# Optimization experiments

Hardware: AMD Instinct MI355X
Metric: run time of the kernel (lower is better)

The kernel has to match this reference:

```python
import jax, jax.numpy as jnp
import numpy as np

FREQ_RES = 100.0 / 256.0
NUM_FILTERS = 6
_CFG = [(0.5, 4.0), (4.0, 8.0), (8.0, 12.0), (12.0, 16.0), (16.0, 24.0), (24.0, 30.0)]
BANDS = [(int(a / FREQ_RES), int(b / FREQ_RES)) for a, b in _CFG]  # (start_bin, end_bin)


def _interp_idx(n_src, n_dst):
    # torch F.interpolate bilinear, align_corners=False, along last dim (T dim is identity since same size)
    j = np.arange(n_dst)
    src = np.maximum((j + 0.5) * n_src / n_dst - 0.5, 0.0)
    x0 = np.floor(src).astype(np.int32)
    x1 = np.minimum(x0 + 1, n_src - 1)
    w = (src - x0).astype(np.float32)
    return x0, x1, w


def _gelu(x):
    return jax.nn.gelu(x, approximate=False)


def _forward(spec, centers, widths, gains, align_w, align_b, fc1_w, fc1_b, fc2_w, fc2_b,
             band_gain, gate_w, gate_b, proj_w, proj_b, bn_gamma, bn_beta, bn_mean, bn_var):
    B, C, T, F = spec.shape
    N = NUM_FILTERS
    band_feats = []
    for i, (s, e) in enumerate(BANDS):
        nb = e - s + 1
        sl = spec[:, :, :, s:e + 1]                       # [B,C,T,nb]
        mu = jax.nn.softplus(centers[i]) + s              # [C,N]
        mu = jnp.clip(mu, s, s + nb - 1)
        std = jnp.clip(jax.nn.softplus(widths[i]) + 1e-3, 0.5, 2.0 * nb / N)
        freqs = jnp.arange(nb, dtype=spec.dtype)          # relative bins [nb]
        g = jnp.exp(-0.5 * ((freqs[None, None, :] - mu[:, :, None]) / std[:, :, None]) ** 2)  # [C,N,nb]
        w = gains[i][:, :, None] * g / (g.sum(-1, keepdims=True) + 1e-6)
        filt = jnp.einsum('bctf,cnf->bctn', sl, w)        # [B,C,T,N]
        aligned = jnp.einsum('bctn,dc->bdtn', filt, align_w[i]) + align_b[i][None, :, None, None]
        band_feats.append(aligned)
    band_stack = jnp.stack(band_feats, axis=1)            # [B,6,C,T,N]
    nb_bands = band_stack.shape[1]
    x = band_stack.reshape(B, nb_bands * C, T, N)
    h = _gelu(jnp.einsum('bktn,ok->botn', x, fc1_w) + fc1_b[None, :, None, None])
    attn = jnp.einsum('botn,ko->bktn', h, fc2_w) + fc2_b[None, :, None, None]
    attn = jax.nn.softmax(attn.reshape(B, nb_bands, C, T, N), axis=1)  # softmax over bands
    band_stack = band_stack * attn * band_gain[None, :, None, None, None]
    enhanced = jnp.zeros_like(spec)
    for i, (s, e) in enumerate(BANDS):
        nb = e - s + 1
        narrow = band_stack[:, i]                         # [B,C,T,N]
        x0, x1, wl = _interp_idx(NUM_FILTERS, nb)
        wl = jnp.asarray(wl, dtype=spec.dtype)
        bf = narrow[..., x0] * (1.0 - wl) + narrow[..., x1] * wl   # [B,C,T,nb]
        enhanced = enhanced.at[:, :, :, s:e + 1].add(bf)
    residual = enhanced - spec
    gate = jax.nn.sigmoid(jnp.einsum('bctf,dc->bdtf', residual, gate_w) + gate_b[None, :, None, None])
    enhanced2 = spec + gate * residual
    y = jnp.einsum('bctf,dc->bdtf', enhanced2, proj_w) + proj_b[None, :, None, None]
    y = (y - bn_mean[None, :, None, None]) / jnp.sqrt(bn_var[None, :, None, None] + 1e-5)
    y = y * bn_gamma[None, :, None, None] + bn_beta[None, :, None, None]
    return _gelu(y)


def setup_inputs() -> dict:
    key = jax.random.key(0)
    ks = jax.random.split(key, 8)
    B, C, T, F, N = 64, 3, 3000, 103, NUM_FILTERS
    spec = jax.random.normal(ks[0], (B, C, T, F), dtype=jnp.float32)
    centers = jnp.stack([jnp.broadcast_to(jnp.linspace(a, b, N, dtype=jnp.float32) / FREQ_RES, (C, N)) for a, b in _CFG])
    widths = jnp.stack([jnp.full((C, N), (b - a) / N / FREQ_RES, dtype=jnp.float32) for a, b in _CFG])
    gains = jnp.ones((6, C, N), jnp.float32)
    align_w = jax.random.normal(ks[1], (6, C, C), dtype=jnp.float32) / np.sqrt(C)
    align_b = jax.random.normal(ks[2], (6, C), dtype=jnp.float32) * 0.02
    inter = 2 * C
    fc1_w = jax.random.normal(ks[3], (inter, 6 * C), dtype=jnp.float32) / np.sqrt(6 * C)
    fc1_b = jnp.zeros((inter,), jnp.float32)
    fc2_w = jax.random.normal(ks[4], (6 * C, inter), dtype=jnp.float32) / np.sqrt(inter)
    fc2_b = jnp.zeros((6 * C,), jnp.float32)
    band_gain = jnp.ones((6,), jnp.float32)
    gate_w = jax.random.normal(ks[5], (C, C), dtype=jnp.float32) / np.sqrt(C)
    gate_b = jnp.zeros((C,), jnp.float32)
    proj_w = jax.random.normal(ks[6], (C, C), dtype=jnp.float32) / np.sqrt(C)
    proj_b = jnp.zeros((C,), jnp.float32)
    bn_gamma = jnp.ones((C,), jnp.float32)
    bn_beta = jnp.zeros((C,), jnp.float32)
    bn_mean = jnp.zeros((C,), jnp.float32)
    bn_var = jnp.ones((C,), jnp.float32)
    return {"spec": spec, "centers": centers, "widths": widths, "gains": gains,
            "align_w": align_w, "align_b": align_b, "fc1_w": fc1_w, "fc1_b": fc1_b,
            "fc2_w": fc2_w, "fc2_b": fc2_b, "band_gain": band_gain,
            "gate_w": gate_w, "gate_b": gate_b, "proj_w": proj_w, "proj_b": proj_b,
            "bn_gamma": bn_gamma, "bn_beta": bn_beta, "bn_mean": bn_mean, "bn_var": bn_var}


def reference(spec, centers, widths, gains, align_w, align_b, fc1_w, fc1_b, fc2_w, fc2_b,
              band_gain, gate_w, gate_b, proj_w, proj_b, bn_gamma, bn_beta, bn_mean, bn_var):
    return _forward(spec, centers, widths, gains, align_w, align_b, fc1_w, fc1_b, fc2_w, fc2_b,
                    band_gain, gate_w, gate_b, proj_w, proj_b, bn_gamma, bn_beta, bn_mean, bn_var)
```

## Files before the change

kernel.cpp:

```cpp
#include <hip/hip_runtime.h>
#include <math.h>

namespace {

constexpr int C_ = 3, T_ = 3000, F_ = 103, NB_ = 6;
constexpr int TT = 20;
constexpr int BS[NB_]  = {1, 10, 20, 30, 40, 61};
constexpr int BNB[NB_] = {10, 11, 11, 11, 22, 16};
constexpr int BOF[NB_] = {0, 10, 21, 32, 43, 65};
constexpr int SPF = 81;
constexpr int PLANE = T_ * F_;
constexpr int SEC = 2064;
constexpr int POOLN = 6320;

__device__ __forceinline__ float softplus_(float x) {
  return fmaxf(x, 0.0f) + log1pf(expf(-fabsf(x)));
}
__device__ __forceinline__ float sigmoid_(float z) {
  return 1.0f / (1.0f + __expf(-z));
}
__device__ __forceinline__ float gelu_(float x) {
  return x * sigmoid_(1.595769122f * x * (1.0f + 0.044715f * x * x));
}

__global__ __launch_bounds__(256)
void sleepband_kernel(const float* __restrict__ spec,
                      const float* __restrict__ centers,
                      const float* __restrict__ widths,
                      const float* __restrict__ gains,
                      const float* __restrict__ align_w,
                      const float* __restrict__ align_b,
                      const float* __restrict__ fc1_w,
                      const float* __restrict__ fc1_b,
                      const float* __restrict__ fc2_w,
                      const float* __restrict__ fc2_b,
                      const float* __restrict__ band_gain,
                      const float* __restrict__ gate_w,
                      const float* __restrict__ gate_b,
                      const float* __restrict__ proj_w,
                      const float* __restrict__ proj_b,
                      const float* __restrict__ bn_gamma,
                      const float* __restrict__ bn_beta,
                      const float* __restrict__ bn_mean,
                      const float* __restrict__ bn_var,
                      float* __restrict__ out)
{
  __shared__ __align__(16) float sPool[POOLN];
  __shared__ float sBand[TT][109];
  __shared__ float sAw[54], sAb[18], sF1[108], sF1b[6], sF2[108], sF2b[18],
                   sBg[6], sGw[9], sGb[3], sPw[9], sPb[3], sBnS[3], sBnO[3];

  const int tid = threadIdx.x;
  const int t0  = blockIdx.x * TT;
  const int b   = blockIdx.y;

  float* sW = sPool + C_ * TT * SPF;

  const float* specB = spec + (size_t)b * C_ * PLANE;
  for (int li = tid; li < C_ * TT * SPF; li += 256) {
    int c   = li / (TT * SPF);
    int rem = li - c * (TT * SPF);
    int tt  = rem / SPF;
    int f   = rem - tt * SPF;
    sPool[li] = specB[(size_t)c * PLANE + (size_t)(t0 + tt) * F_ + f];
  }

  if (tid < 54)  sAw[tid]  = align_w[tid];
  if (tid < 18)  sAb[tid]  = align_b[tid];
  if (tid < 108) sF1[tid]  = fc1_w[tid];
  if (tid < 6)   sF1b[tid] = fc1_b[tid];
  if (tid < 108) sF2[tid]  = fc2_w[tid];
  if (tid < 18)  sF2b[tid] = fc2_b[tid];
  if (tid < 6)   sBg[tid]  = band_gain[tid];
  if (tid < 9)   sGw[tid]  = gate_w[tid];
  if (tid < 3)   sGb[tid]  = gate_b[tid];
  if (tid < 9)   sPw[tid]  = proj_w[tid];
  if (tid < 3)   sPb[tid]  = proj_b[tid];
  if (tid < 3) {
    float sc = bn_gamma[tid] / sqrtf(bn_var[tid] + 1e-5f);
    sBnS[tid] = sc;
    sBnO[tid] = bn_beta[tid] - bn_mean[tid] * sc;
  }

  if (tid >= 128 && tid < 128 + 108) {
    int q = tid - 128;
    int i = q / 18;
    int p = q - i * 18;
    int s = BS[i], nb = BNB[i];
    float mu = softplus_(centers[q]) + (float)s;
    mu = fminf(fmaxf(mu, (float)s), (float)(s + nb - 1));
    float sd = softplus_(widths[q]) + 0.001f;
    sd = fminf(fmaxf(sd, 0.5f), 2.0f * (float)nb / 6.0f);
    float sum = 0.0f;
    for (int f = 0; f < nb; ++f) {
      float d = ((float)f - mu) / sd;
      sum += __expf(-0.5f * d * d);
    }
    float sc = gains[q] / (sum + 1e-6f);
    float* wrow = &sW[BOF[i] * 18 + p * nb];
    for (int f = 0; f < nb; ++f) {
      float d = ((float)f - mu) / sd;
      wrow[f] = sc * __expf(-0.5f * d * d);
    }
  }
  __syncthreads();

  for (int task = tid; task < 18 * TT; task += 256) {
    int p  = task / TT;
    int tt = task - p * TT;
    int c  = p / 6;
    int n  = p - c * 6;
    const float* srowb = &sPool[(c * TT + tt) * SPF];
    #pragma unroll
    for (int i = 0; i < NB_; ++i) {
      const float* wrow = &sW[BOF[i] * 18 + p * BNB[i]];
      const float* srow = srowb + BS[i];
      float acc = 0.0f;
      #pragma unroll
      for (int f = 0; f < BNB[i]; ++f) acc += srow[f] * wrow[f];
      sBand[tt][(i * 3 + c) * 6 + n] = acc;
    }
  }
  __syncthreads();

  if (tid < 6 * TT) {
    int n  = tid / TT;
    int tt = tid - n * TT;
    float al[18];
    #pragma unroll
    for (int i = 0; i < 6; ++i) {
      float f0 = sBand[tt][(i * 3 + 0) * 6 + n];
      float f1 = sBand[tt][(i * 3 + 1) * 6 + n];
      float f2 = sBand[tt][(i * 3 + 2) * 6 + n];
      #pragma unroll
      for (int d = 0; d < 3; ++d)
        al[i * 3 + d] = sAw[i * 9 + d * 3 + 0] * f0 + sAw[i * 9 + d * 3 + 1] * f1 +
                        sAw[i * 9 + d * 3 + 2] * f2 + sAb[i * 3 + d];
    }
    float h[6];
    #pragma unroll
    for (int o = 0; o < 6; ++o) {
      float acc = sF1b[o];
      #pragma unroll
      for (int k = 0; k < 18; ++k) acc += sF1[o * 18 + k] * al[k];
      h[o] = gelu_(acc);
    }
    float at[18];
    #pragma unroll
    for (int k = 0; k < 18; ++k) {
      float acc = sF2b[k];
      #pragma unroll
      for (int o = 0; o < 6; ++o) acc += sF2[k * 6 + o] * h[o];
      at[k] = acc;
    }
    #pragma unroll
    for (int c = 0; c < 3; ++c) {
      float m = at[c];
      #pragma unroll
      for (int i = 1; i < 6; ++i) m = fmaxf(m, at[i * 3 + c]);
      float e[6], ssum = 0.0f;
      #pragma unroll
      for (int i = 0; i < 6; ++i) { e[i] = __expf(at[i * 3 + c] - m); ssum += e[i]; }
      float inv = 1.0f / ssum;
      #pragma unroll
      for (int i = 0; i < 6; ++i)
        sBand[tt][(i * 3 + c) * 6 + n] = al[i * 3 + c] * (e[i] * inv) * sBg[i];
    }
  }
  __syncthreads();

  if (tid < C_ * TT) {
    const int c  = tid / TT;
    const int tt = tid - c * TT;
    float bnd[36];
    #pragma unroll
    for (int i = 0; i < 6; ++i)
      #pragma unroll
      for (int n = 0; n < 6; ++n)
        bnd[i * 6 + n] = sBand[tt][(i * 3 + c) * 6 + n];
    float* row = &sPool[c * SEC + tt * F_];
    row[0] = 0.0f;
    float carry = 0.0f;
    #pragma unroll
    for (int i = 0; i < NB_; ++i) {
      #pragma unroll
      for (int j = 0; j < BNB[i]; ++j) {
        float src = ((float)j + 0.5f) * 6.0f / (float)BNB[i] - 0.5f;
        src = src > 0.0f ? src : 0.0f;
        int   x0 = (int)src;
        int   x1 = (x0 < 5) ? x0 + 1 : 5;
        float wl = src - (float)x0;
        float v  = bnd[i * 6 + x0] * (1.0f - wl) + bnd[i * 6 + x1] * wl;
        if (j == 0) v += carry;
        if (i < NB_ - 1 && j == BNB[i] - 1) carry = v;
        else row[BS[i] + j] = v;
      }
    }
    #pragma unroll
    for (int f = 77; f < F_; ++f) row[f] = 0.0f;
  }
  __syncthreads();

  float gw[9], pw[9], gb3[3], pb3[3], bs3[3], bo3[3];
  #pragma unroll
  for (int k = 0; k < 9; ++k) { gw[k] = sGw[k]; pw[k] = sPw[k]; }
  #pragma unroll
  for (int k = 0; k < 3; ++k) { gb3[k] = sGb[k]; pb3[k] = sPb[k]; bs3[k] = sBnS[k]; bo3[k] = sBnO[k]; }

  const float* sp0 = specB + (size_t)t0 * F_;
  float* outB = out + (size_t)b * C_ * PLANE + (size_t)t0 * F_;
  for (int e4 = tid; e4 < (TT * F_) / 4; e4 += 256) {
    const int e = e4 * 4;
    const float4 sA = *(const float4*)(sp0 + e);
    const float4 sB = *(const float4*)(sp0 + PLANE + e);
    const float4 sC = *(const float4*)(sp0 + 2 * PLANE + e);
    const float4 eA = *(const float4*)&sPool[0 * SEC + e];
    const float4 eB = *(const float4*)&sPool[1 * SEC + e];
    const float4 eC = *(const float4*)&sPool[2 * SEC + e];
    float4 oA, oB, oC;
    const float* sAp = (const float*)&sA; const float* sBp = (const float*)&sB;
    const float* sCp = (const float*)&sC;
    const float* eAp = (const float*)&eA; const float* eBp = (const float*)&eB;
    const float* eCp = (const float*)&eC;
    float* oAp = (float*)&oA; float* oBp = (float*)&oB; float* oCp = (float*)&oC;
    #pragma unroll
    for (int j = 0; j < 4; ++j) {
      float sv0 = sAp[j], sv1 = sBp[j], sv2 = sCp[j];
      float r0 = eAp[j] - sv0, r1 = eBp[j] - sv1, r2 = eCp[j] - sv2;
      float e20 = sv0 + sigmoid_(gw[0] * r0 + gw[1] * r1 + gw[2] * r2 + gb3[0]) * r0;
      float e21 = sv1 + sigmoid_(gw[3] * r0 + gw[4] * r1 + gw[5] * r2 + gb3[1]) * r1;
      float e22 = sv2 + sigmoid_(gw[6] * r0 + gw[7] * r1 + gw[8] * r2 + gb3[2]) * r2;
      float y0 = (pw[0] * e20 + pw[1] * e21 + pw[2] * e22 + pb3[0]) * bs3[0] + bo3[0];
      float y1 = (pw[3] * e20 + pw[4] * e21 + pw[5] * e22 + pb3[1]) * bs3[1] + bo3[1];
      float y2 = (pw[6] * e20 + pw[7] * e21 + pw[8] * e22 + pb3[2]) * bs3[2] + bo3[2];
      oAp[j] = gelu_(y0); oBp[j] = gelu_(y1); oCp[j] = gelu_(y2);
    }
    *(float4*)(outB + e) = oA;
    *(float4*)(outB + PLANE + e) = oB;
    *(float4*)(outB + 2 * PLANE + e) = oC;
  }
}

}

extern "C" void kernel_launch(void* const* d_in, const int* in_sizes, int n_in,
                              void* d_out, int out_size, void* d_ws, size_t ws_size,
                              hipStream_t stream) {
  (void)n_in; (void)out_size; (void)d_ws; (void)ws_size;
  const int B = in_sizes[0] / (C_ * T_ * F_);
  dim3 grid(T_ / TT, B);
  sleepband_kernel<<<grid, 256, 0, stream>>>(
      (const float*)d_in[0],  (const float*)d_in[1],  (const float*)d_in[2],
      (const float*)d_in[3],  (const float*)d_in[4],  (const float*)d_in[5],
      (const float*)d_in[6],  (const float*)d_in[7],  (const float*)d_in[8],
      (const float*)d_in[9],  (const float*)d_in[10], (const float*)d_in[11],
      (const float*)d_in[12], (const float*)d_in[13], (const float*)d_in[14],
      (const float*)d_in[15], (const float*)d_in[16], (const float*)d_in[17],
      (const float*)d_in[18], (float*)d_out);
}
```

Before: 246.9 us.

## Hoist Gaussian filter build into prep kernel, shrink time tile, fold BN into projection

A separate single-block prep kernel now builds the per-band Gaussian filter weights once into the workspace, and every main block copies them instead of recomputing softplus/exp per block. The time tile drops from 20 to 12 rows, which shrinks shared memory and raises the block count, and launch bounds request 6 blocks per CU for higher occupancy. Batch-norm scale and offset are folded into the projection weights and bias to remove per-element multiplies. The trade-offs are an extra kernel launch plus a dependency on the workspace, and more blocks that each reload the small weight tables and the three spec planes.

After: 279.6 us. 1.13x slower.

```diff
diff --git a/kernel.cpp b/kernel.cpp
--- a/kernel.cpp
+++ b/kernel.cpp
@@ -4,16 +4,17 @@
 namespace {
 
 constexpr int C_ = 3, T_ = 3000, F_ = 103, NB_ = 6;
-constexpr int TT = 20;
+constexpr int TT = 12;
 constexpr int BS[NB_]  = {1, 10, 20, 30, 40, 61};
 constexpr int BNB[NB_] = {10, 11, 11, 11, 22, 16};
 constexpr int BOF[NB_] = {0, 10, 21, 32, 43, 65};
 constexpr int SPF = 81;
 constexpr int PLANE = T_ * F_;
-constexpr int SEC = 2064;
-constexpr int POOLN = 6320;
-
-__device__ __forceinline__ float softplus_(float x) {
+constexpr int SEC = TT * F_;
+constexpr int WTOT = 81 * 18;
+constexpr int POOLN = C_ * TT * SPF + WTOT;
+
+__device__ __forceinline__ float softplus_full_(float x) {
   return fmaxf(x, 0.0f) + log1pf(expf(-fabsf(x)));
 }
 __device__ __forceinline__ float sigmoid_(float z) {
@@ -23,11 +24,37 @@
   return x * sigmoid_(1.595769122f * x * (1.0f + 0.044715f * x * x));
 }
 
-__global__ __launch_bounds__(256)
+__global__ __launch_bounds__(128)
+void prep_kernel(const float* __restrict__ centers,
+                 const float* __restrict__ widths,
+                 const float* __restrict__ gains,
+                 float* __restrict__ wfilt)
+{
+  const int q = threadIdx.x;
+  if (q >= 108) return;
+  int i = q / 18;
+  int p = q - i * 18;
+  int s = BS[i], nb = BNB[i];
+  float mu = softplus_full_(centers[q]) + (float)s;
+  mu = fminf(fmaxf(mu, (float)s), (float)(s + nb - 1));
+  float sd = softplus_full_(widths[q]) + 0.001f;
+  sd = fminf(fmaxf(sd, 0.5f), 2.0f * (float)nb / 6.0f);
+  float sum = 0.0f;
+  for (int f = 0; f < nb; ++f) {
+    float d = ((float)f - mu) / sd;
+    sum += __expf(-0.5f * d * d);
+  }
+  float sc = gains[q] / (sum + 1e-6f);
+  float* wrow = &wfilt[BOF[i] * 18 + p * nb];
+  for (int f = 0; f < nb; ++f) {
+    float d = ((float)f - mu) / sd;
+    wrow[f] = sc * __expf(-0.5f * d * d);
+  }
+}
+
+__global__ __launch_bounds__(256, 6)
 void sleepband_kernel(const float* __restrict__ spec,
-                      const float* __restrict__ centers,
-                      const float* __restrict__ widths,
-                      const float* __restrict__ gains,
+                      const float* __restrict__ wfilt,
                       const float* __restrict__ align_w,
                       const float* __restrict__ align_b,
                       const float* __restrict__ fc1_w,
@@ -48,7 +75,7 @@
   __shared__ __align__(16) float sPool[POOLN];
   __shared__ float sBand[TT][109];
   __shared__ float sAw[54], sAb[18], sF1[108], sF1b[6], sF2[108], sF2b[18],
-                   sBg[6], sGw[9], sGb[3], sPw[9], sPb[3], sBnS[3], sBnO[3];
+                   sBg[6], sGw[9], sGb[3], sPw[9], sPb[3];
 
   const int tid = threadIdx.x;
   const int t0  = blockIdx.x * TT;
@@ -64,6 +91,7 @@
     int f   = rem - tt * SPF;
     sPool[li] = specB[(size_t)c * PLANE + (size_t)(t0 + tt) * F_ + f];
   }
+  for (int k = tid; k < WTOT; k += 256) sW[k] = wfilt[k];
 
   if (tid < 54)  sAw[tid]  = align_w[tid];
   if (tid < 18)  sAb[tid]  = align_b[tid];
@@ -74,40 +102,20 @@
   if (tid < 6)   sBg[tid]  = band_gain[tid];
   if (tid < 9)   sGw[tid]  = gate_w[tid];
   if (tid < 3)   sGb[tid]  = gate_b[tid];
-  if (tid < 9)   sPw[tid]  = proj_w[tid];
-  if (tid < 3)   sPb[tid]  = proj_b[tid];
+  if (tid < 9) {
+    int d = tid / 3;
+    float sc = bn_gamma[d] * __frsqrt_rn(bn_var[d] + 1e-5f);
+    sPw[tid] = proj_w[tid] * sc;
+  }
   if (tid < 3) {
-    float sc = bn_gamma[tid] / sqrtf(bn_var[tid] + 1e-5f);
-    sBnS[tid] = sc;
-    sBnO[tid] = bn_beta[tid] - bn_mean[tid] * sc;
-  }
-
-  if (tid >= 128 && tid < 128 + 108) {
-    int q = tid - 128;
-    int i = q / 18;
-    int p = q - i * 18;
-    int s = BS[i], nb = BNB[i];
-    float mu = softplus_(centers[q]) + (float)s;
-    mu = fminf(fmaxf(mu, (float)s), (float)(s + nb - 1));
-    float sd = softplus_(widths[q]) + 0.001f;
-    sd = fminf(fmaxf(sd, 0.5f), 2.0f * (float)nb / 6.0f);
-    float sum = 0.0f;
-    for (int f = 0; f < nb; ++f) {
-      float d = ((float)f - mu) / sd;
-      sum += __expf(-0.5f * d * d);
-    }
-    float sc = gains[q] / (sum + 1e-6f);
-    float* wrow = &sW[BOF[i] * 18 + p * nb];
-    for (int f = 0; f < nb; ++f) {
-      float d = ((float)f - mu) / sd;
-      wrow[f] = sc * __expf(-0.5f * d * d);
-    }
-  }
-  __syncthreads();
-
-  for (int task = tid; task < 18 * TT; task += 256) {
-    int p  = task / TT;
-    int tt = task - p * TT;
+    float sc = bn_gamma[tid] * __frsqrt_rn(bn_var[tid] + 1e-5f);
+    sPb[tid] = (proj_b[tid] - bn_mean[tid]) * sc + bn_beta[tid];
+  }
+  __syncthreads();
+
+  if (tid < 18 * TT) {
+    int p  = tid / TT;
+    int tt = tid - p * TT;
     int c  = p / 6;
     int n  = p - c * 6;
     const float* srowb = &sPool[(c * TT + tt) * SPF];
@@ -201,15 +209,15 @@
   }
   __syncthreads();
 
-  float gw[9], pw[9], gb3[3], pb3[3], bs3[3], bo3[3];
+  float gw[9], pw[9], gb3[3], pb3[3];
   #pragma unroll
   for (int k = 0; k < 9; ++k) { gw[k] = sGw[k]; pw[k] = sPw[k]; }
   #pragma unroll
-  for (int k = 0; k < 3; ++k) { gb3[k] = sGb[k]; pb3[k] = sPb[k]; bs3[k] = sBnS[k]; bo3[k] = sBnO[k]; }
+  for (int k = 0; k < 3; ++k) { gb3[k] = sGb[k]; pb3[k] = sPb[k]; }
 
   const float* sp0 = specB + (size_t)t0 * F_;
   float* outB = out + (size_t)b * C_ * PLANE + (size_t)t0 * F_;
-  for (int e4 = tid; e4 < (TT * F_) / 4; e4 += 256) {
+  for (int e4 = tid; e4 < SEC / 4; e4 += 256) {
     const int e = e4 * 4;
     const float4 sA = *(const float4*)(sp0 + e);
     const float4 sB = *(const float4*)(sp0 + PLANE + e);
@@ -230,9 +238,9 @@
       float e20 = sv0 + sigmoid_(gw[0] * r0 + gw[1] * r1 + gw[2] * r2 + gb3[0]) * r0;
       float e21 = sv1 + sigmoid_(gw[3] * r0 + gw[4] * r1 + gw[5] * r2 + gb3[1]) * r1;
       float e22 = sv2 + sigmoid_(gw[6] * r0 + gw[7] * r1 + gw[8] * r2 + gb3[2]) * r2;
-      float y0 = (pw[0] * e20 + pw[1] * e21 + pw[2] * e22 + pb3[0]) * bs3[0] + bo3[0];
-      float y1 = (pw[3] * e20 + pw[4] * e21 + pw[5] * e22 + pb3[1]) * bs3[1] + bo3[1];
-      float y2 = (pw[6] * e20 + pw[7] * e21 + pw[8] * e22 + pb3[2]) * bs3[2] + bo3[2];
+      float y0 = pw[0] * e20 + pw[1] * e21 + pw[2] * e22 + pb3[0];
+      float y1 = pw[3] * e20 + pw[4] * e21 + pw[5] * e22 + pb3[1];
+      float y2 = pw[6] * e20 + pw[7] * e21 + pw[8] * e22 + pb3[2];
       oAp[j] = gelu_(y0); oBp[j] = gelu_(y1); oCp[j] = gelu_(y2);
     }
     *(float4*)(outB + e) = oA;
@@ -246,12 +254,15 @@
 extern "C" void kernel_launch(void* const* d_in, const int* in_sizes, int n_in,
                               void* d_out, int out_size, void* d_ws, size_t ws_size,
                               hipStream_t stream) {
-  (void)n_in; (void)out_size; (void)d_ws; (void)ws_size;
+  (void)n_in; (void)out_size; (void)ws_size;
   const int B = in_sizes[0] / (C_ * T_ * F_);
+  float* wfilt = (float*)d_ws;
+  prep_kernel<<<1, 128, 0, stream>>>(
+      (const float*)d_in[1], (const float*)d_in[2], (const float*)d_in[3], wfilt);
   dim3 grid(T_ / TT, B);
   sleepband_kernel<<<grid, 256, 0, stream>>>(
-      (const float*)d_in[0],  (const float*)d_in[1],  (const float*)d_in[2],
-      (const float*)d_in[3],  (const float*)d_in[4],  (const float*)d_in[5],
+      (const float*)d_in[0],  wfilt,
+      (const float*)d_in[4],  (const float*)d_in[5],
       (const float*)d_in[6],  (const float*)d_in[7],  (const float*)d_in[8],
       (const float*)d_in[9],  (const float*)d_in[10], (const float*)d_in[11],
       (const float*)d_in[12], (const float*)d_in[13], (const float*)d_in[14],
```
